# Optimization experiments

Hardware: AMD Instinct MI355X
Metric: run time of the kernel (lower is better)

## Reference

```python
import jax, jax.numpy as jnp
import numpy as np
import math

DIM = 1024
N_HEADS = 16
HEAD_DIM = DIM // N_HEADS


def rope(x):
    # x: [B, H, S, D] with D == HEAD_DIM, interleaved even/odd rotation
    S = x.shape[-2]
    D = x.shape[-1]
    pos = jnp.arange(S, dtype=x.dtype)[:, None]              # [S, 1]
    dim = jnp.arange(D // 2, dtype=x.dtype)[None, :]         # [1, D/2]
    theta = pos / jnp.exp(2.0 * dim / D * math.log(10000.0))  # [S, D/2]
    sin = jnp.sin(theta)[None, None]                          # [1,1,S,D/2]
    cos = jnp.cos(theta)[None, None]
    x1 = x[..., ::2]
    x2 = x[..., 1::2]
    out1 = x1 * cos - x2 * sin
    out2 = x1 * sin + x2 * cos
    # interleave back: stack on last axis then flatten pairs
    return jnp.stack([out1, out2], axis=-1).reshape(x.shape)


def setup_inputs() -> dict:
    key = jax.random.key(0)
    ks = jax.random.split(key, 9)
    B, S = 2, 2048
    s = 1.0 / math.sqrt(DIM)
    inp = {
        "x": jax.random.normal(ks[0], (B, S, DIM), dtype=jnp.float32),
        "wq": jax.random.normal(ks[1], (DIM, DIM), dtype=jnp.float32) * s,
        "bq": jnp.zeros((DIM,), dtype=jnp.float32),
        "wk": jax.random.normal(ks[2], (DIM, DIM), dtype=jnp.float32) * s,
        "bk": jnp.zeros((DIM,), dtype=jnp.float32),
        "wv": jax.random.normal(ks[3], (DIM, DIM), dtype=jnp.float32) * s,
        "bv": jnp.zeros((DIM,), dtype=jnp.float32),
        "wo": jax.random.normal(ks[4], (DIM, DIM), dtype=jnp.float32) * s,
        "bo": jnp.zeros((DIM,), dtype=jnp.float32),
    }
    return inp


def reference(x, wq, bq, wk, bk, wv, bv, wo, bo):
    B, S, _ = x.shape
    # torch Linear: y = x @ W^T + b
    def proj(w, b):
        y = jnp.einsum('bsd,ed->bse', x, w) + b
        return y.reshape(B, S, N_HEADS, HEAD_DIM).transpose(0, 2, 1, 3)  # [B,H,S,Dh]
    q = rope(proj(wq, bq))
    k = rope(proj(wk, bk))
    v = proj(wv, bv)
    score = jnp.einsum('bhqd,bhkd->bhqk', q, k) / math.sqrt(HEAD_DIM)
    causal = jnp.tril(jnp.ones((S, S), dtype=bool))
    score = jnp.where(causal[None, None], score, -jnp.inf)
    attn = jax.nn.softmax(score, axis=-1)
    out = jnp.einsum('bhqk,bhkd->bhqd', attn, v)
    out = out.transpose(0, 2, 1, 3).reshape(B, S, DIM)
    return jnp.einsum('bsd,ed->bse', out, wo) + bo
```

## Files before the change

kernel.cpp:

```cpp
#include <hip/hip_runtime.h>
#include <cstdint>
#include <cstddef>
#include <cmath>


typedef __bf16 bf16_t;
typedef __bf16 bf16x8 __attribute__((ext_vector_type(8)));
typedef __bf16 bf16x4 __attribute__((ext_vector_type(4)));
typedef float  f32x4  __attribute__((ext_vector_type(4)));

#define DEVFN __device__ __forceinline__

static constexpr int Bn  = 2;
static constexpr int S   = 2048;
static constexpr int DIM = 1024;
static constexpr int NH  = 16;
static constexpr int HD  = 64;
static constexpr int Mrows = Bn * S;

DEVFN f32x4 mfma16(bf16x8 a, bf16x8 b, f32x4 c) {
  return __builtin_amdgcn_mfma_f32_16x16x32_bf16(a, b, c, 0, 0, 0);
}

DEVFN void gl_lds16(const bf16_t* g, bf16_t* l) {
  __builtin_amdgcn_global_load_lds(
      (const __attribute__((address_space(1))) unsigned*)g,
      (__attribute__((address_space(3))) unsigned*)l, 16, 0, 0);
}

DEVFN float fast_exp2(float x) { return exp2f(x); }

__global__ __launch_bounds__(256) void k_prep(
    const float* __restrict__ x, const float* __restrict__ wq,
    const float* __restrict__ wk, const float* __restrict__ wv,
    const float* __restrict__ wo, bf16_t* __restrict__ xb,
    bf16_t* __restrict__ wqb, bf16_t* __restrict__ wkb,
    bf16_t* __restrict__ wvb, bf16_t* __restrict__ wob,
    float2* __restrict__ tab) {
  const int bid = blockIdx.x;
  if (bid < 8192) {
    const float* src;
    bf16_t* dst;
    size_t base;
    if (bid < 4096) {
      src = x; dst = xb; base = (size_t)bid << 10;
    } else {
      int wsel = (bid - 4096) >> 10;
      src = wsel == 0 ? wq : wsel == 1 ? wk : wsel == 2 ? wv : wo;
      dst = wsel == 0 ? wqb : wsel == 1 ? wkb : wsel == 2 ? wvb : wob;
      base = (size_t)((bid - 4096) & 1023) << 10;
    }
    size_t i = base + (size_t)threadIdx.x * 4;
    float4 v = *(const float4*)(src + i);
    bf16x4 o = { (bf16_t)v.x, (bf16_t)v.y, (bf16_t)v.z, (bf16_t)v.w };
    *(bf16x4*)(dst + i) = o;
  } else {
    int i = (bid - 8192) * 256 + threadIdx.x;
    int s = i >> 5, d = i & 31;
    float th = (float)s * expf((float)d * -0.2878231366f);
    tab[i] = make_float2(cosf(th), sinf(th));
  }
}

__global__ __launch_bounds__(256) void k_rope2(bf16_t* __restrict__ q,
                                               bf16_t* __restrict__ k,
                                               const float2* __restrict__ tab,
                                               float sq) {
  const int bid = blockIdx.x;
  bf16_t* X = bid < 2048 ? q : k;
  const float scale = bid < 2048 ? sq : 1.0f;
  int i = (bid & 2047) * 256 + threadIdx.x;
  int row = i >> 7;
  int s = row & (S - 1);
  int p0 = (i & 7) << 2;
  bf16x8 v = *(bf16x8*)(X + (size_t)i * 8);
  bf16x8 o;
#pragma unroll
  for (int j = 0; j < 4; ++j) {
    float x1 = (float)v[2 * j], x2 = (float)v[2 * j + 1];
    float2 cs = tab[s * 32 + p0 + j];
    o[2 * j]     = (bf16_t)((x1 * cs.x - x2 * cs.y) * scale);
    o[2 * j + 1] = (bf16_t)((x1 * cs.y + x2 * cs.x) * scale);
  }
  *(bf16x8*)(X + (size_t)i * 8) = o;
}

__global__ __launch_bounds__(256) void k_trans(const bf16_t* __restrict__ Vin,
                                               bf16_t* __restrict__ VT) {
  __shared__ __align__(16) bf16_t tile[64][72];
  int s0 = blockIdx.x * 64, bh = blockIdx.y;
  int b = bh >> 4, h = bh & 15;
  int t = threadIdx.x;
#pragma unroll
  for (int it = 0; it < 2; ++it) {
    int sl = (t >> 3) + it * 32, d0 = (t & 7) << 3;
    *(bf16x8*)&tile[sl][d0] =
        *(const bf16x8*)(Vin + (size_t)(b * S + s0 + sl) * DIM + h * HD + d0);
  }
  __syncthreads();
  int d = t >> 2, c0 = (t & 3) * 16;
  bf16_t buf[16];
#pragma unroll
  for (int j = 0; j < 16; ++j) buf[j] = tile[c0 + j][d];
  bf16_t* op = VT + ((size_t)bh * HD + d) * S + s0 + c0;
  *(bf16x8*)op = *(bf16x8*)&buf[0];
  *(bf16x8*)(op + 8) = *(bf16x8*)&buf[8];
}

DEVFN void stage64(const bf16_t* __restrict__ A, const bf16_t* __restrict__ Bw,
                   bf16_t* Al, bf16_t* Bl, int m0, int n0, int k0, int t,
                   int w) {
#pragma unroll
  for (int ld = 0; ld < 4; ++ld) {
    int c = t + ld * 256;
    int row = c >> 3;
    int j = ((c & 7) ^ (row & 7)) << 3;
    bf16_t* dstA = Al + (size_t)(w * 64 + ld * 256) * 8;
    bf16_t* dstB = Bl + (size_t)(w * 64 + ld * 256) * 8;
    gl_lds16(A + (size_t)(m0 + row) * DIM + k0 + j, dstA);
    gl_lds16(Bw + (size_t)(n0 + row) * DIM + k0 + j, dstB);
  }
}

__global__ __launch_bounds__(256) void k_gemm_qkv(
    const bf16_t* __restrict__ A, const bf16_t* __restrict__ Wall,
    const float* __restrict__ c0, const float* __restrict__ c1,
    const float* __restrict__ c2, bf16_t* __restrict__ Oq,
    bf16_t* __restrict__ Ok, bf16_t* __restrict__ Ov_) {
  __shared__ __align__(16) bf16_t Al[128 * 64];
  __shared__ __align__(16) bf16_t Bl[128 * 64];
  const int t = threadIdx.x, w = t >> 6, l = t & 63;
  const int lr = l & 15, lc = l >> 4;
  const int lid = blockIdx.x;
  const int xcd = lid & 7, s = lid >> 3;
  const int my = ((xcd >> 1) << 3) + (s & 7);
  const int nx = (xcd & 1) * 12 + (s >> 3);
  const int m0 = my * 128, n0g = nx * 128;
  const int z = n0g >> 10, n0l = n0g & 1023;
  const int wr = w >> 1, wc = w & 1;
  f32x4 acc[4][4] = {};

  for (int k0 = 0; k0 < DIM; k0 += 64) {
    __syncthreads();
    stage64(A, Wall, Al, Bl, m0, n0g, k0, t, w);
    asm volatile("s_waitcnt vmcnt(0)" ::: "memory");
    __syncthreads();
    bf16x8 af[2][4], bfr[2][4];
#pragma unroll
    for (int ks = 0; ks < 2; ++ks) {
#pragma unroll
      for (int mi = 0; mi < 4; ++mi) {
        int row = wr * 64 + mi * 16 + lr;
        int off = ((ks * 4 + lc) << 4) ^ ((row & 7) << 4);
        af[ks][mi] = *(const bf16x8*)((const char*)Al + row * 128 + off);
      }
#pragma unroll
      for (int ni = 0; ni < 4; ++ni) {
        int row = wc * 64 + ni * 16 + lr;
        int off = ((ks * 4 + lc) << 4) ^ ((row & 7) << 4);
        bfr[ks][ni] = *(const bf16x8*)((const char*)Bl + row * 128 + off);
      }
    }
    __builtin_amdgcn_s_setprio(1);
#pragma unroll
    for (int ks = 0; ks < 2; ++ks)
#pragma unroll
      for (int mi = 0; mi < 4; ++mi)
#pragma unroll
        for (int ni = 0; ni < 4; ++ni)
          acc[mi][ni] = mfma16(af[ks][mi], bfr[ks][ni], acc[mi][ni]);
    __builtin_amdgcn_s_setprio(0);
  }

  bf16_t* Ov = z == 0 ? Oq : (z == 1 ? Ok : Ov_);
  const float* bias = z == 0 ? c0 : (z == 1 ? c1 : c2);
#pragma unroll
  for (int ni = 0; ni < 4; ++ni) {
    const int col = n0l + wc * 64 + ni * 16 + lr;
    const float bv = bias[col];
#pragma unroll
    for (int mi = 0; mi < 4; ++mi)
#pragma unroll
      for (int r = 0; r < 4; ++r) {
        int row = m0 + wr * 64 + mi * 16 + lc * 4 + r;
        Ov[(size_t)row * DIM + col] = (bf16_t)(acc[mi][ni][r] + bv);
      }
  }
}

__global__ __launch_bounds__(256) void k_gemm_out(
    const bf16_t* __restrict__ A, const bf16_t* __restrict__ Bw,
    const float* __restrict__ bias, float* __restrict__ Ov) {
  __shared__ __align__(16) bf16_t Al[128 * 64];
  __shared__ __align__(16) bf16_t Bl[64 * 64];
  const int t = threadIdx.x, w = t >> 6, l = t & 63;
  const int lr = l & 15, lc = l >> 4;
  const int lid = blockIdx.x;
  const int xcd = lid & 7, s = lid >> 3;
  const int my = ((xcd >> 1) << 3) + (s & 7);
  const int nx = (xcd & 1) * 8 + (s >> 3);
  const int m0 = my * 128, n0 = nx * 64;
  f32x4 acc[2][4] = {};

  for (int k0 = 0; k0 < DIM; k0 += 64) {
    __syncthreads();
#pragma unroll
    for (int ld = 0; ld < 4; ++ld) {
      int c = t + ld * 256;
      int row = c >> 3;
      int j = ((c & 7) ^ (row & 7)) << 3;
      gl_lds16(A + (size_t)(m0 + row) * DIM + k0 + j,
               Al + (size_t)(w * 64 + ld * 256) * 8);
    }
#pragma unroll
    for (int ld = 0; ld < 2; ++ld) {
      int c = t + ld * 256;
      int row = c >> 3;
      int j = ((c & 7) ^ (row & 7)) << 3;
      gl_lds16(Bw + (size_t)(n0 + row) * DIM + k0 + j,
               Bl + (size_t)(w * 64 + ld * 256) * 8);
    }
    asm volatile("s_waitcnt vmcnt(0)" ::: "memory");
    __syncthreads();
    bf16x8 af[2][2], bfr[2][4];
#pragma unroll
    for (int ks = 0; ks < 2; ++ks) {
#pragma unroll
      for (int mi = 0; mi < 2; ++mi) {
        int row = w * 32 + mi * 16 + lr;
        int off = ((ks * 4 + lc) << 4) ^ ((row & 7) << 4);
        af[ks][mi] = *(const bf16x8*)((const char*)Al + row * 128 + off);
      }
#pragma unroll
      for (int ni = 0; ni < 4; ++ni) {
        int row = ni * 16 + lr;
        int off = ((ks * 4 + lc) << 4) ^ ((row & 7) << 4);
        bfr[ks][ni] = *(const bf16x8*)((const char*)Bl + row * 128 + off);
      }
    }
    __builtin_amdgcn_s_setprio(1);
#pragma unroll
    for (int ks = 0; ks < 2; ++ks)
#pragma unroll
      for (int mi = 0; mi < 2; ++mi)
#pragma unroll
        for (int ni = 0; ni < 4; ++ni)
          acc[mi][ni] = mfma16(af[ks][mi], bfr[ks][ni], acc[mi][ni]);
    __builtin_amdgcn_s_setprio(0);
  }

#pragma unroll
  for (int ni = 0; ni < 4; ++ni) {
    int col = n0 + ni * 16 + lr;
    float bv = bias[col];
#pragma unroll
    for (int mi = 0; mi < 2; ++mi)
#pragma unroll
      for (int r = 0; r < 4; ++r) {
        int row = m0 + w * 32 + mi * 16 + lc * 4 + r;
        Ov[(size_t)row * DIM + col] = acc[mi][ni][r] + bv;
      }
  }
}

DEVFN void stage_kv(const bf16_t* __restrict__ Kc,
                    const bf16_t* __restrict__ VT, bf16_t* Kb, bf16_t* Vb,
                    int b, int bh, int h, int k0, int tid, int w) {
#pragma unroll
  for (int ld = 0; ld < 2; ++ld) {
    int c = tid + ld * 256;
    int row = c >> 3;
    int j = ((c & 7) ^ (row & 7)) << 3;
    bf16_t* dstK = Kb + (size_t)(w * 64 + ld * 256) * 8;
    bf16_t* dstV = Vb + (size_t)(w * 64 + ld * 256) * 8;
    gl_lds16(Kc + (size_t)(b * S + k0 + row) * DIM + h * HD + j, dstK);
    gl_lds16(VT + ((size_t)bh * HD + row) * S + k0 + j, dstV);
  }
}

__global__ __launch_bounds__(256) void k_attn(const bf16_t* __restrict__ Q,
                                              const bf16_t* __restrict__ Kc,
                                              const bf16_t* __restrict__ VT,
                                              bf16_t* __restrict__ O) {
  __shared__ __align__(16) bf16_t Kl[64 * 64];
  __shared__ __align__(16) bf16_t Vl[64 * 64];
  __shared__ __align__(16) bf16_t Pl[4][16 * 64];
  const int tid = threadIdx.x, w = tid >> 6, l = tid & 63;
  const int lr = l & 15, lc = l >> 4;
  const int lid = blockIdx.x;
  const int xcd = lid & 7;
  const int rest = lid >> 3;
  const int t_ord = rest >> 2;
  const int hh = rest & 3;
  const int tile = 31 - t_ord;
  const int bh = xcd * 4 + hh;
  const int b = bh >> 4, h = bh & 15;
  char* Pw = (char*)&Pl[w][0];

  const int q0 = tile * 64;
  const int nt = tile + 1;

  bf16x8 qf[2];
  {
    const bf16_t* qp =
        Q + (size_t)(b * S + q0 + w * 16 + lr) * DIM + h * HD + lc * 8;
    qf[0] = *(const bf16x8*)qp;
    qf[1] = *(const bf16x8*)(qp + 32);
  }
  f32x4 o[4] = {};
  float m_run = -INFINITY;
  float rowsum = 0.f;

#pragma unroll 1
  for (int it = 0; it < nt; ++it) {
    stage_kv(Kc, VT, &Kl[0], &Vl[0], b, bh, h, it * 64, tid, w);
    asm volatile("s_waitcnt vmcnt(0)" ::: "memory");
    __builtin_amdgcn_s_barrier();
    __builtin_amdgcn_sched_barrier(0);

    f32x4 s[4] = {};
    __builtin_amdgcn_s_setprio(1);
#pragma unroll
    for (int ks = 0; ks < 2; ++ks) {
#pragma unroll
      for (int ni = 0; ni < 4; ++ni) {
        int row = ni * 16 + lr;
        int off = (ks * 64 + lc * 16) ^ ((row & 7) << 4);
        bf16x8 kf = *(const bf16x8*)((const char*)Kl + row * 128 + off);
        s[ni] = mfma16(kf, qf[ks], s[ni]);
      }
    }
    __builtin_amdgcn_s_setprio(0);

    if (it == tile) {
      const int qloc = w * 16 + lr;
#pragma unroll
      for (int ni = 0; ni < 4; ++ni)
#pragma unroll
        for (int r = 0; r < 4; ++r)
          if (ni * 16 + lc * 4 + r > qloc) s[ni][r] = -INFINITY;
    }

    float m01 = fmaxf(fmaxf(s[0][0], s[0][1]), fmaxf(s[0][2], s[0][3]));
    float m23 = fmaxf(fmaxf(s[1][0], s[1][1]), fmaxf(s[1][2], s[1][3]));
    float m45 = fmaxf(fmaxf(s[2][0], s[2][1]), fmaxf(s[2][2], s[2][3]));
    float m67 = fmaxf(fmaxf(s[3][0], s[3][1]), fmaxf(s[3][2], s[3][3]));
    float pm = fmaxf(fmaxf(m01, m23), fmaxf(m45, m67));
    pm = fmaxf(pm, __shfl_xor(pm, 16));
    pm = fmaxf(pm, __shfl_xor(pm, 32));

    if (__ballot(pm > m_run + 8.f)) {
      float mn = fmaxf(m_run, pm);
      float alpha = fast_exp2(m_run - mn);
      m_run = mn;
      rowsum *= alpha;
#pragma unroll
      for (int r = 0; r < 4; ++r) {
        float aq = __shfl(alpha, lc * 4 + r);
#pragma unroll
        for (int ni = 0; ni < 4; ++ni) o[ni][r] *= aq;
      }
    }

    float rs = 0.f;
#pragma unroll
    for (int ni = 0; ni < 4; ++ni) {
      float p0 = fast_exp2(s[ni][0] - m_run);
      float p1 = fast_exp2(s[ni][1] - m_run);
      float p2 = fast_exp2(s[ni][2] - m_run);
      float p3 = fast_exp2(s[ni][3] - m_run);
      rs += (p0 + p1) + (p2 + p3);
      bf16x4 pb = { (bf16_t)p0, (bf16_t)p1, (bf16_t)p2, (bf16_t)p3 };
      *(bf16x4*)(Pw + (lr * 128 + ((ni * 32 + lc * 8) ^ ((lr & 7) << 4)))) =
          pb;
    }
    rs += __shfl_xor(rs, 16);
    rs += __shfl_xor(rs, 32);
    rowsum += rs;

    __builtin_amdgcn_s_setprio(1);
#pragma unroll
    for (int ks = 0; ks < 2; ++ks) {
      int off = ks * 64 + lc * 16;
      bf16x8 pa = *(const bf16x8*)(Pw + lr * 128 + (off ^ ((lr & 7) << 4)));
#pragma unroll
      for (int ni = 0; ni < 4; ++ni) {
        int vrow = ni * 16 + lr;
        bf16x8 vb = *(const bf16x8*)((const char*)Vl + vrow * 128 +
                                     (off ^ ((vrow & 7) << 4)));
        o[ni] = mfma16(pa, vb, o[ni]);
      }
    }
    __builtin_amdgcn_s_setprio(0);

    __builtin_amdgcn_s_barrier();
  }

  float inv[4];
#pragma unroll
  for (int r = 0; r < 4; ++r) inv[r] = 1.0f / __shfl(rowsum, lc * 4 + r);
#pragma unroll
  for (int ni = 0; ni < 4; ++ni)
#pragma unroll
    for (int r = 0; r < 4; ++r) {
      int qr = q0 + w * 16 + lc * 4 + r;
      float v = o[ni][r] * inv[r];
      O[(size_t)(b * S + qr) * DIM + h * HD + ni * 16 + lr] = (bf16_t)v;
    }
}

extern "C" void kernel_launch(void* const* d_in, const int* in_sizes, int n_in,
                              void* d_out, int out_size, void* d_ws,
                              size_t ws_size, hipStream_t stream) {
  const float* x  = (const float*)d_in[0];
  const float* wq = (const float*)d_in[1];
  const float* bq = (const float*)d_in[2];
  const float* wk = (const float*)d_in[3];
  const float* bk = (const float*)d_in[4];
  const float* wv = (const float*)d_in[5];
  const float* bv = (const float*)d_in[6];
  const float* wo = (const float*)d_in[7];
  const float* bo = (const float*)d_in[8];

  const size_t MD = (size_t)Mrows * DIM;
  const size_t WD = (size_t)DIM * DIM;
  bf16_t* W = (bf16_t*)d_ws;
  bf16_t* x_bf  = W;
  bf16_t* wq_bf = x_bf + MD;
  bf16_t* wk_bf = wq_bf + WD;
  bf16_t* wv_bf = wk_bf + WD;
  bf16_t* wo_bf = wv_bf + WD;
  bf16_t* q_lin = wo_bf + WD;
  bf16_t* k_lin = q_lin + MD;
  bf16_t* v_lin = k_lin + MD;
  bf16_t* vT    = v_lin + MD;
  float2* tab   = (float2*)(vT + MD);
  bf16_t* attn_out = x_bf;

  k_prep<<<8448, 256, 0, stream>>>(x, wq, wk, wv, wo, x_bf, wq_bf, wk_bf,
                                   wv_bf, wo_bf, tab);

  k_gemm_qkv<<<768, 256, 0, stream>>>(x_bf, wq_bf, bq, bk, bv, q_lin, k_lin,
                                      v_lin);

  k_rope2<<<4096, 256, 0, stream>>>(q_lin, k_lin, tab,
                                    0.125f * 1.4426950408889634f);
  k_trans<<<dim3(S / 64, Bn * NH), 256, 0, stream>>>(v_lin, vT);

  k_attn<<<1024, 256, 0, stream>>>(q_lin, k_lin, vT, attn_out);

  k_gemm_out<<<512, 256, 0, stream>>>(attn_out, wo_bf, bo, (float*)d_out);
}
```

Baseline: 124.6 us.

## Process 128 query rows per attention block to reuse staged K/V tiles

Each attention block now covers two 64-row query groups (128 rows total) rather than one. Every K/V tile staged into LDS therefore feeds twice as many QK and PV MFMAs, and the grid shrinks from 1024 to 512 blocks. Per-group masking and softmax state are tracked separately, and the first group skips the final tile. The cost is more registers per thread, fewer blocks to spread across CUs, and coarser causal load balancing.

```diff
diff --git a/kernel.cpp b/kernel.cpp
--- a/kernel.cpp
+++ b/kernel.cpp
@@ -284,7 +284,7 @@
                                               bf16_t* __restrict__ O) {
   __shared__ __align__(16) bf16_t Kl[64 * 64];
   __shared__ __align__(16) bf16_t Vl[64 * 64];
-  __shared__ __align__(16) bf16_t Pl[4][16 * 64];
+  __shared__ __align__(16) bf16_t Pl[4][2][16 * 64];
   const int tid = threadIdx.x, w = tid >> 6, l = tid & 63;
   const int lr = l & 15, lc = l >> 4;
   const int lid = blockIdx.x;
@@ -292,55 +292,31 @@
   const int rest = lid >> 3;
   const int t_ord = rest >> 2;
   const int hh = rest & 3;
-  const int tile = 31 - t_ord;
+  const int t128 = 15 - t_ord;
   const int bh = xcd * 4 + hh;
   const int b = bh >> 4, h = bh & 15;
-  char* Pw = (char*)&Pl[w][0];
-
-  const int q0 = tile * 64;
-  const int nt = tile + 1;
-
-  bf16x8 qf[2];
+  char* Pw0 = (char*)&Pl[w][0][0];
+  char* Pw1 = (char*)&Pl[w][1][0];
+
+  const int q0 = t128 * 128;
+  const int nt = 2 * t128 + 2;
+
+  bf16x8 qf0[2], qf1[2];
   {
     const bf16_t* qp =
         Q + (size_t)(b * S + q0 + w * 16 + lr) * DIM + h * HD + lc * 8;
-    qf[0] = *(const bf16x8*)qp;
-    qf[1] = *(const bf16x8*)(qp + 32);
-  }
-  f32x4 o[4] = {};
-  float m_run = -INFINITY;
-  float rowsum = 0.f;
-
-#pragma unroll 1
-  for (int it = 0; it < nt; ++it) {
-    stage_kv(Kc, VT, &Kl[0], &Vl[0], b, bh, h, it * 64, tid, w);
-    asm volatile("s_waitcnt vmcnt(0)" ::: "memory");
-    __builtin_amdgcn_s_barrier();
-    __builtin_amdgcn_sched_barrier(0);
-
-    f32x4 s[4] = {};
-    __builtin_amdgcn_s_setprio(1);
-#pragma unroll
-    for (int ks = 0; ks < 2; ++ks) {
-#pragma unroll
-      for (int ni = 0; ni < 4; ++ni) {
-        int row = ni * 16 + lr;
-        int off = (ks * 64 + lc * 16) ^ ((row & 7) << 4);
-        bf16x8 kf = *(const bf16x8*)((const char*)Kl + row * 128 + off);
-        s[ni] = mfma16(kf, qf[ks], s[ni]);
-      }
-    }
-    __builtin_amdgcn_s_setprio(0);
-
-    if (it == tile) {
-      const int qloc = w * 16 + lr;
-#pragma unroll
-      for (int ni = 0; ni < 4; ++ni)
-#pragma unroll
-        for (int r = 0; r < 4; ++r)
-          if (ni * 16 + lc * 4 + r > qloc) s[ni][r] = -INFINITY;
-    }
-
+    qf0[0] = *(const bf16x8*)qp;
+    qf0[1] = *(const bf16x8*)(qp + 32);
+    const bf16_t* qp1 = qp + (size_t)64 * DIM;
+    qf1[0] = *(const bf16x8*)qp1;
+    qf1[1] = *(const bf16x8*)(qp1 + 32);
+  }
+  f32x4 o0[4] = {}, o1[4] = {};
+  float m0r = -INFINITY, m1r = -INFINITY;
+  float rs0t = 0.f, rs1t = 0.f;
+
+  auto softmax_g = [&](f32x4(&s)[4], float& m_run, float& rowsum,
+                       f32x4(&o)[4], char* Pwg) {
     float m01 = fmaxf(fmaxf(s[0][0], s[0][1]), fmaxf(s[0][2], s[0][3]));
     float m23 = fmaxf(fmaxf(s[1][0], s[1][1]), fmaxf(s[1][2], s[1][3]));
     float m45 = fmaxf(fmaxf(s[2][0], s[2][1]), fmaxf(s[2][2], s[2][3]));
@@ -348,7 +324,6 @@
     float pm = fmaxf(fmaxf(m01, m23), fmaxf(m45, m67));
     pm = fmaxf(pm, __shfl_xor(pm, 16));
     pm = fmaxf(pm, __shfl_xor(pm, 32));
-
     if (__ballot(pm > m_run + 8.f)) {
       float mn = fmaxf(m_run, pm);
       float alpha = fast_exp2(m_run - mn);
@@ -361,7 +336,6 @@
         for (int ni = 0; ni < 4; ++ni) o[ni][r] *= aq;
       }
     }
-
     float rs = 0.f;
 #pragma unroll
     for (int ni = 0; ni < 4; ++ni) {
@@ -371,41 +345,103 @@
       float p3 = fast_exp2(s[ni][3] - m_run);
       rs += (p0 + p1) + (p2 + p3);
       bf16x4 pb = { (bf16_t)p0, (bf16_t)p1, (bf16_t)p2, (bf16_t)p3 };
-      *(bf16x4*)(Pw + (lr * 128 + ((ni * 32 + lc * 8) ^ ((lr & 7) << 4)))) =
+      *(bf16x4*)(Pwg + (lr * 128 + ((ni * 32 + lc * 8) ^ ((lr & 7) << 4)))) =
           pb;
     }
     rs += __shfl_xor(rs, 16);
     rs += __shfl_xor(rs, 32);
     rowsum += rs;
-
+  };
+
+  auto mask_diag = [&](f32x4(&s)[4]) {
+    const int qloc = w * 16 + lr;
+#pragma unroll
+    for (int ni = 0; ni < 4; ++ni)
+#pragma unroll
+      for (int r = 0; r < 4; ++r)
+        if (ni * 16 + lc * 4 + r > qloc) s[ni][r] = -INFINITY;
+  };
+
+#pragma unroll 1
+  for (int it = 0; it < nt; ++it) {
+    stage_kv(Kc, VT, &Kl[0], &Vl[0], b, bh, h, it * 64, tid, w);
+    asm volatile("s_waitcnt vmcnt(0)" ::: "memory");
+    __builtin_amdgcn_s_barrier();
+    __builtin_amdgcn_sched_barrier(0);
+
+    const bool g0a = (it < nt - 1);
+
+    f32x4 s0[4] = {}, s1[4] = {};
     __builtin_amdgcn_s_setprio(1);
 #pragma unroll
     for (int ks = 0; ks < 2; ++ks) {
-      int off = ks * 64 + lc * 16;
-      bf16x8 pa = *(const bf16x8*)(Pw + lr * 128 + (off ^ ((lr & 7) << 4)));
 #pragma unroll
       for (int ni = 0; ni < 4; ++ni) {
-        int vrow = ni * 16 + lr;
-        bf16x8 vb = *(const bf16x8*)((const char*)Vl + vrow * 128 +
-                                     (off ^ ((vrow & 7) << 4)));
-        o[ni] = mfma16(pa, vb, o[ni]);
+        int row = ni * 16 + lr;
+        int off = (ks * 64 + lc * 16) ^ ((row & 7) << 4);
+        bf16x8 kf = *(const bf16x8*)((const char*)Kl + row * 128 + off);
+        s0[ni] = mfma16(kf, qf0[ks], s0[ni]);
+        s1[ni] = mfma16(kf, qf1[ks], s1[ni]);
       }
     }
     __builtin_amdgcn_s_setprio(0);
 
+    if (it == nt - 2) mask_diag(s0);
+    if (it == nt - 1) mask_diag(s1);
+
+    if (g0a) softmax_g(s0, m0r, rs0t, o0, Pw0);
+    softmax_g(s1, m1r, rs1t, o1, Pw1);
+
+    __builtin_amdgcn_s_setprio(1);
+    if (g0a) {
+#pragma unroll
+      for (int ks = 0; ks < 2; ++ks) {
+        int off = ks * 64 + lc * 16;
+        bf16x8 pa0 = *(const bf16x8*)(Pw0 + lr * 128 + (off ^ ((lr & 7) << 4)));
+        bf16x8 pa1 = *(const bf16x8*)(Pw1 + lr * 128 + (off ^ ((lr & 7) << 4)));
+#pragma unroll
+        for (int ni = 0; ni < 4; ++ni) {
+          int vrow = ni * 16 + lr;
+          bf16x8 vb = *(const bf16x8*)((const char*)Vl + vrow * 128 +
+                                       (off ^ ((vrow & 7) << 4)));
+          o0[ni] = mfma16(pa0, vb, o0[ni]);
+          o1[ni] = mfma16(pa1, vb, o1[ni]);
+        }
+      }
+    } else {
+#pragma unroll
+      for (int ks = 0; ks < 2; ++ks) {
+        int off = ks * 64 + lc * 16;
+        bf16x8 pa1 = *(const bf16x8*)(Pw1 + lr * 128 + (off ^ ((lr & 7) << 4)));
+#pragma unroll
+        for (int ni = 0; ni < 4; ++ni) {
+          int vrow = ni * 16 + lr;
+          bf16x8 vb = *(const bf16x8*)((const char*)Vl + vrow * 128 +
+                                       (off ^ ((vrow & 7) << 4)));
+          o1[ni] = mfma16(pa1, vb, o1[ni]);
+        }
+      }
+    }
+    __builtin_amdgcn_s_setprio(0);
+
     __builtin_amdgcn_s_barrier();
   }
 
-  float inv[4];
-#pragma unroll
-  for (int r = 0; r < 4; ++r) inv[r] = 1.0f / __shfl(rowsum, lc * 4 + r);
+  float inv0[4], inv1[4];
+#pragma unroll
+  for (int r = 0; r < 4; ++r) {
+    inv0[r] = 1.0f / __shfl(rs0t, lc * 4 + r);
+    inv1[r] = 1.0f / __shfl(rs1t, lc * 4 + r);
+  }
 #pragma unroll
   for (int ni = 0; ni < 4; ++ni)
 #pragma unroll
     for (int r = 0; r < 4; ++r) {
       int qr = q0 + w * 16 + lc * 4 + r;
-      float v = o[ni][r] * inv[r];
-      O[(size_t)(b * S + qr) * DIM + h * HD + ni * 16 + lr] = (bf16_t)v;
+      O[(size_t)(b * S + qr) * DIM + h * HD + ni * 16 + lr] =
+          (bf16_t)(o0[ni][r] * inv0[r]);
+      O[(size_t)(b * S + qr + 64) * DIM + h * HD + ni * 16 + lr] =
+          (bf16_t)(o1[ni][r] * inv1[r]);
     }
 }
 
@@ -447,7 +483,7 @@
                                     0.125f * 1.4426950408889634f);
   k_trans<<<dim3(S / 64, Bn * NH), 256, 0, stream>>>(v_lin, vT);
 
-  k_attn<<<1024, 256, 0, stream>>>(q_lin, k_lin, vT, attn_out);
+  k_attn<<<512, 256, 0, stream>>>(q_lin, k_lin, vT, attn_out);
 
   k_gemm_out<<<512, 256, 0, stream>>>(attn_out, wo_bf, bo, (float*)d_out);
 }
```

After: 146.8 us. +17.8%, slower.
